# Optimization experiments

Measured on AMD Instinct MI355X. Metric: run time of the kernel, lower is better.

## Reference

```python
import jax, jax.numpy as jnp
import numpy as np

N_E = 1024
E_DIM = 256
BETA = 0.25
DECAY = 0.99
EPS = 1e-5


def setup_inputs() -> dict:
    key = jax.random.key(0)
    k1, k2 = jax.random.split(key)
    z = jax.random.normal(k1, (16, E_DIM, 64, 64), dtype=jnp.float32)
    # embedding.weight.data.uniform_(-1/n_e, 1/n_e)
    weight = jax.random.uniform(k2, (N_E, E_DIM), dtype=jnp.float32,
                                minval=-1.0 / N_E, maxval=1.0 / N_E)
    cluster_size = jnp.zeros((N_E,), dtype=jnp.float32)
    embedding_avg = weight  # clone of initial weight
    return {"z": z, "weight": weight, "cluster_size": cluster_size,
            "embedding_avg": embedding_avg}


def reference(z, weight, cluster_size, embedding_avg):
    B, C, H, W = z.shape  # C == e_dim
    zp = jnp.transpose(z, (0, 2, 3, 1))          # [B,H,W,C]
    zf = zp.reshape(-1, C)                       # [N, C], N = B*H*W

    # ||z||^2 + ||e||^2 - 2 z e^T  -> [N, n_e]
    d = (jnp.sum(zf * zf, axis=1, keepdims=True)
         + jnp.sum(weight * weight, axis=1)
         - 2.0 * jnp.matmul(zf, weight.T))
    idx = jnp.argmin(d, axis=1)                  # [N] int

    z_q = weight[idx].reshape(zp.shape)          # [B,H,W,C]

    # EMA codebook update (training branch), computed with scatter-sums
    n_e = weight.shape[0]
    counts = jax.ops.segment_sum(jnp.ones(zf.shape[0], dtype=zf.dtype),
                                 idx, num_segments=n_e)        # encodings.sum(0)
    new_cluster_size = cluster_size * DECAY + (1.0 - DECAY) * counts
    n = jnp.sum(new_cluster_size)
    cs_smoothed = (new_cluster_size + EPS) / (n + n_e * EPS) * n
    dw = jax.ops.segment_sum(zf, idx, num_segments=n_e)        # encodings.T @ zf
    new_embedding_avg = embedding_avg * DECAY + (1.0 - DECAY) * dw
    new_weight = new_embedding_avg / cs_smoothed[:, None]

    loss = BETA * jnp.mean((jax.lax.stop_gradient(z_q) - zp) ** 2)
    z_q_st = zp + jax.lax.stop_gradient(z_q - zp)   # straight-through
    out = jnp.transpose(z_q_st, (0, 3, 1, 2))        # back to NCHW
    return out, loss, idx, new_cluster_size, new_embedding_avg, new_weight
```

## Files before the change

### kernel.cpp

```cpp
#include <hip/hip_runtime.h>
#include <hip/hip_bf16.h>

typedef unsigned short ushort_t;
typedef __attribute__((ext_vector_type(8))) _Float16 half8;
typedef __attribute__((ext_vector_type(4))) _Float16 half4;
typedef __attribute__((ext_vector_type(4))) float f32x4;

#define NB    16
#define NC    256
#define NHW   4096
#define NPIX  65536
#define NE    1024
#define BETA  0.25f
#define DECAY 0.99f
#define EPS_  1e-5f
#define GAP_FLAG 1.25e-4f

#define OFF_LOSS 16777216
#define OFF_IDXF 16777217
#define OFF_NCS  16842753
#define OFF_NEA  16843777
#define OFF_NW   17105921

#define WS_WSUM  0
#define WS_CSSM  1024
#define WS_LPART 2048
#define WS_CNT   4096
#define WS_FLAGS 4128
#define WS_LIST  6176
#define WS_WF16  40960
#define WS_ZF16  (WS_WF16 + 131072)
#define WS_IDXI  (WS_ZF16 + 8388608)
#define WS_CCNT  (WS_IDXI + 65536)
#define WS_OFFS  (WS_CCNT + 1024)
#define WS_CUR   (WS_OFFS + 1024)
#define WS_SORT  (WS_CUR + 1024)
#define WS_END   (WS_SORT + 65536)

__device__ __forceinline__ float sq_nofma(float x) {
    float s = x * x;
    asm volatile("" : "+v"(s));
    return s;
}

__device__ __forceinline__ float np_pair128_sq(const float* __restrict__ a) {
    float r[8];
    #pragma unroll
    for (int m = 0; m < 8; ++m) r[m] = sq_nofma(a[m]);
    for (int i = 8; i < 128; i += 8) {
        #pragma unroll
        for (int m = 0; m < 8; ++m) r[m] += sq_nofma(a[i + m]);
    }
    return ((r[0] + r[1]) + (r[2] + r[3])) + ((r[4] + r[5]) + (r[6] + r[7]));
}

__device__ __forceinline__ void gload16(const void* g, void* ldsp) {
    __builtin_amdgcn_global_load_lds((const __attribute__((address_space(1))) unsigned int*)g,
                                     (__attribute__((address_space(3))) unsigned int*)ldsp,
                                     16, 0, 0);
}

__global__ __launch_bounds__(64) void wsum_kernel(const float* __restrict__ w,
                                                  float* __restrict__ wsum,
                                                  float* __restrict__ ncs,
                                                  int* __restrict__ cnt,
                                                  int* __restrict__ ccount,
                                                  float* __restrict__ lpart) {
    int j = blockIdx.x * 64 + threadIdx.x;
    const float* wr = w + (size_t)j * NC;
    wsum[j] = np_pair128_sq(wr) + np_pair128_sq(wr + 128);
    ncs[j] = 0.0f;
    ccount[j] = 0;
    lpart[j] = 0.0f;
    lpart[j + 1024] = 0.0f;
    if (j == 0) cnt[0] = 0;
}

__global__ __launch_bounds__(256) void wpack_kernel(const float* __restrict__ w,
                                                    _Float16* __restrict__ wf) {
    int i = blockIdx.x * 256 + threadIdx.x;
    wf[i] = (_Float16)(w[i] * 1024.0f);
}

__global__ __launch_bounds__(256) void zpack_kernel(const float* __restrict__ z,
                                                    _Float16* __restrict__ zf) {
    __shared__ float zs[64 * 65];
    const int t = threadIdx.x;
    const int P0 = blockIdx.x * 64;
    const int b = P0 >> 12, hw0 = P0 & (NHW - 1);
    const int K0 = blockIdx.y * 64;
    const int hw = t & 63, cq = t >> 6;
    const float* zb = z + (size_t)b * (NC * NHW) + hw0 + hw;
    #pragma unroll
    for (int i = 0; i < 16; ++i) {
        int kl = cq * 16 + i;
        zs[hw * 65 + kl] = zb[(size_t)(K0 + kl) * NHW];
    }
    __syncthreads();
    const int p = t >> 2, kq = t & 3;
    size_t obase = (size_t)(P0 + p) * NC + K0 + kq * 16;
    #pragma unroll
    for (int h2 = 0; h2 < 2; ++h2) {
        half8 v;
        #pragma unroll
        for (int j2 = 0; j2 < 8; ++j2)
            v[j2] = (_Float16)zs[p * 65 + kq * 16 + h2 * 8 + j2];
        *(half8*)&zf[obase + h2 * 8] = v;
    }
}

__global__ __launch_bounds__(512) void gemm2_kernel(const _Float16* __restrict__ wf,
                                                    const _Float16* __restrict__ zf,
                                                    const float* __restrict__ wsum,
                                                    float* __restrict__ idxf,
                                                    int* __restrict__ idxi,
                                                    ushort_t* __restrict__ list,
                                                    int* __restrict__ cnt,
                                                    float* __restrict__ ncs,
                                                    int* __restrict__ ccount) {
    __shared__ __align__(16) char smem[147456];
    _Float16* zt = (_Float16*)smem;
    _Float16* wt = (_Float16*)(smem + 131072);
    float* bvx = (float*)(smem + 131072);
    float* svx = bvx + 512;
    int*   bix = (int*)(svx + 512);
    int*   h   = (int*)smem;

    const int t = threadIdx.x;
    const int l = t & 63;
    const int w = t >> 6;
    const int P0 = blockIdx.x * 256;
    const int wc = w >> 2;
    const int wp = w & 3;

    const int sdest = w * 512 + l * 8;
    const int swrow = w * 16 + (l >> 2);
    const _Float16* wsrc0 = wf + (size_t)swrow * 256 + (((l & 3) ^ ((l >> 3) & 3)) * 8);
    int aoff[4];
    #pragma unroll
    for (int m = 0; m < 4; ++m) {
        int row = wc * 64 + m * 16 + (l & 15);
        int g = (l >> 4) ^ ((row >> 1) & 3);
        aoff[m] = row * 32 + g * 8;
    }
    int bbase[4], bx32[4];
    #pragma unroll
    for (int n = 0; n < 4; ++n) {
        int row = wp * 64 + n * 16 + (l & 15);
        int r3 = row & 7;
        bbase[n] = row * 256 + (((l >> 4) ^ (r3 & 3)) * 8);
        bx32[n] = (r3 >> 2) * 32;
    }

    #pragma unroll
    for (int i = 0; i < 16; ++i) {
        int row = w * 32 + i * 2 + (l >> 5);
        int gc = (l & 31) ^ (row & 7);
        gload16(zf + (size_t)(P0 + row) * NC + gc * 8,
                &zt[w * 8192 + i * 512 + l * 8]);
    }
    gload16(wsrc0, &wt[sdest]);

    float rbv2[4], rsv2[4];
    int   rbi2[4];
    #pragma unroll
    for (int n = 0; n < 4; ++n) { rbv2[n] = 3.4e38f; rsv2[n] = 3.4e38f; rbi2[n] = 0; }

    __syncthreads();

    for (int ct = 0; ct < 8; ++ct) {
        const _Float16* wsrc_ct = wsrc0 + ct * 32768;
        f32x4 acc[4][4];
        #pragma unroll
        for (int m = 0; m < 4; ++m)
            #pragma unroll
            for (int n = 0; n < 4; ++n)
                #pragma unroll
                for (int e = 0; e < 4; ++e) acc[m][n][e] = 0.0f;

        #pragma unroll
        for (int ks = 0; ks < 8; ++ks) {
            if (ct < 7 || ks < 7) {
                const _Float16* src = (ks < 7) ? (wsrc_ct + (ks + 1) * 32)
                                               : (wsrc_ct + 32768);
                gload16(src, &wt[((ks & 1) ^ 1) * 4096 + sdest]);
            }
            __builtin_amdgcn_s_setprio(1);
            half8 a[4], b[4];
            #pragma unroll
            for (int m = 0; m < 4; ++m)
                a[m] = *(const half8*)&wt[(ks & 1) * 4096 + aoff[m]];
            #pragma unroll
            for (int n = 0; n < 4; ++n)
                b[n] = *(const half8*)&zt[bbase[n] + ((ks * 32) ^ bx32[n])];
            #pragma unroll
            for (int m = 0; m < 4; ++m)
                #pragma unroll
                for (int n = 0; n < 4; ++n)
                    acc[m][n] = __builtin_amdgcn_mfma_f32_16x16x32_f16(a[m], b[n], acc[m][n], 0, 0, 0);
            __builtin_amdgcn_s_setprio(0);
            __syncthreads();
        }

        #pragma unroll
        for (int m = 0; m < 4; ++m) {
            float4 env = *(const float4*)&wsum[ct * 128 + wc * 64 + m * 16 + (l >> 4) * 4];
            const float* en = &env.x;
            #pragma unroll
            for (int n = 0; n < 4; ++n)
                #pragma unroll
                for (int r = 0; r < 4; ++r) {
                    float s = en[r] - acc[m][n][r] * 0.001953125f;
                    int code = ct * 128 + wc * 64 + m * 16 + (l >> 4) * 4 + r;
                    if (s < rbv2[n]) { rsv2[n] = rbv2[n]; rbv2[n] = s; rbi2[n] = code; }
                    else if (s < rsv2[n]) rsv2[n] = s;
                }
        }
    }

    #pragma unroll
    for (int n = 0; n < 4; ++n) {
        float bv = rbv2[n], sv = rsv2[n];
        int bi = rbi2[n];
        #pragma unroll
        for (int x = 16; x <= 32; x <<= 1) {
            float v2 = __shfl_xor(bv, x);
            float s2 = __shfl_xor(sv, x);
            int   i2 = __shfl_xor(bi, x);
            if (v2 < bv || (v2 == bv && i2 < bi)) { sv = fminf(bv, s2); bv = v2; bi = i2; }
            else sv = fminf(sv, v2);
        }
        if ((l >> 4) == 0) {
            int lp = wp * 64 + n * 16 + l;
            bvx[wc * 256 + lp] = bv;
            svx[wc * 256 + lp] = sv;
            bix[wc * 256 + lp] = bi;
        }
    }
    h[t] = 0;
    h[t + 512] = 0;
    __syncthreads();
    if (t < 256) {
        float bv = bvx[t], sv = svx[t];
        int bi = bix[t];
        float v2 = bvx[256 + t], s2 = svx[256 + t];
        int i2 = bix[256 + t];
        if (v2 < bv || (v2 == bv && i2 < bi)) { sv = fminf(bv, s2); bv = v2; bi = i2; }
        else sv = fminf(sv, v2);
        int pix = P0 + t;
        idxf[pix] = (float)bi;
        idxi[pix] = bi;
        atomicAdd(&h[bi], 1);
        if (sv - bv < GAP_FLAG) {
            int pos = atomicAdd(cnt, 1);
            list[pos] = (ushort_t)pix;
        }
    }
    __syncthreads();
    {
        int v = h[t];
        if (v) { atomicAdd(&ncs[t], (float)v); atomicAdd(&ccount[t], v); }
        v = h[t + 512];
        if (v) { atomicAdd(&ncs[t + 512], (float)v); atomicAdd(&ccount[t + 512], v); }
    }
}

__global__ __launch_bounds__(256) void argmin_kernel(const float* __restrict__ z,
                                                     const float* __restrict__ w,
                                                     const float* __restrict__ enorm,
                                                     float* __restrict__ idxf,
                                                     int* __restrict__ idxi,
                                                     unsigned long long* __restrict__ flags) {
    __shared__ __align__(16) float smem[64 * 68 + 128 * 68];
    float* zt = smem;
    float* wt = smem + 64 * 68;
    const int t = threadIdx.x;
    const int pr = t & 7;
    const int cr = t >> 3;
    const int P0 = blockIdx.x * 64;
    const int b = P0 >> 12;
    const int hw0 = P0 & (NHW - 1);
    const float* zb = z + (size_t)b * (NC * NHW) + hw0;
    float bestv[8], secv[8];
    int besti[8];
    #pragma unroll
    for (int i = 0; i < 8; ++i) { bestv[i] = 3.4e38f; secv[i] = 3.4e38f; besti[i] = 0; }
    for (int cc = 0; cc < 8; ++cc) {
        float acc[8][4];
        #pragma unroll
        for (int i = 0; i < 8; ++i)
            #pragma unroll
            for (int j = 0; j < 4; ++j) acc[i][j] = 0.0f;
        for (int kc = 0; kc < 4; ++kc) {
            {
                int p = t & 63;
                int k0 = (t >> 6) * 16;
                int f2 = ((p >> 3) & 3) << 2;
                #pragma unroll
                for (int i = 0; i < 16; ++i) {
                    int k = k0 + i;
                    zt[p * 68 + (k ^ f2)] = zb[(size_t)(kc * 64 + k) * NHW + p];
                }
            }
            {
                #pragma unroll
                for (int i = 0; i < 8; ++i) {
                    int f = t + 256 * i;
                    int jj = f >> 4;
                    int k4 = f & 15;
                    float4 v = *(const float4*)&w[(size_t)(cc * 128 + jj) * NC + kc * 64 + k4 * 4];
                    *(float4*)&wt[jj * 68 + k4 * 4] = v;
                }
            }
            __syncthreads();
            #pragma unroll 2
            for (int k = 0; k < 64; k += 4) {
                float4 za[8], wb[4];
                #pragma unroll
                for (int i = 0; i < 8; ++i)
                    za[i] = *(float4*)&zt[(pr + 8 * i) * 68 + (k ^ ((i & 3) << 2))];
                #pragma unroll
                for (int j = 0; j < 4; ++j)
                    wb[j] = *(float4*)&wt[(cr + 32 * j) * 68 + k];
                #pragma unroll
                for (int i = 0; i < 8; ++i)
                    #pragma unroll
                    for (int j = 0; j < 4; ++j)
                        acc[i][j] += za[i].x * wb[j].x + za[i].y * wb[j].y +
                                     za[i].z * wb[j].z + za[i].w * wb[j].w;
            }
            __syncthreads();
        }
        #pragma unroll
        for (int j = 0; j < 4; ++j) {
            int code = cc * 128 + cr + 32 * j;
            float enj = enorm[code];
            #pragma unroll
            for (int i = 0; i < 8; ++i) {
                float s = enj - 2.0f * acc[i][j];
                if (s < bestv[i]) { secv[i] = bestv[i]; bestv[i] = s; besti[i] = code; }
                else if (s < secv[i]) secv[i] = s;
            }
        }
    }
    float* rv = smem;
    int* ri = (int*)(smem + 2048);
    float* rs = smem + 4096;
    #pragma unroll
    for (int i = 0; i < 8; ++i) {
        int p = pr + 8 * i;
        rv[p * 32 + cr] = bestv[i];
        ri[p * 32 + cr] = besti[i];
        rs[p * 32 + cr] = secv[i];
    }
    __syncthreads();
    if (t < 64) {
        int p = t;
        float bv = rv[p * 32], sv = rs[p * 32];
        int bi = ri[p * 32];
        for (int s2 = 1; s2 < 32; ++s2) {
            float v = rv[p * 32 + s2];
            float v2 = rs[p * 32 + s2];
            int ii = ri[p * 32 + s2];
            if (v < bv) { sv = bv; bv = v; bi = ii; }
            else {
                if (v < sv) sv = v;
                if (v == bv && ii < bi) bi = ii;
            }
            if (v2 < sv) sv = v2;
        }
        idxf[P0 + p] = (float)bi;
        idxi[P0 + p] = bi;
        unsigned long long mask = __ballot((sv - bv) < GAP_FLAG);
        if (t == 0) flags[blockIdx.x] = mask;
    }
}

__global__ __launch_bounds__(256) void gather_kernel(const unsigned long long* __restrict__ flags,
                                                     ushort_t* __restrict__ list,
                                                     int* __restrict__ cnt) {
    int p = blockIdx.x * 256 + threadIdx.x;
    unsigned long long m = flags[p >> 6];
    if ((m >> (p & 63)) & 1ULL) {
        int pos = atomicAdd(cnt, 1);
        list[pos] = (ushort_t)p;
    }
}

__global__ __launch_bounds__(1024) void hist_kernel(const int* __restrict__ idxi,
                                                    float* __restrict__ ncs) {
    __shared__ int h[NE];
    int t = threadIdx.x;
    h[t] = 0;
    __syncthreads();
    int gid = blockIdx.x * 1024 + t;
    #pragma unroll
    for (int i = 0; i < 4; ++i) atomicAdd(&h[idxi[gid + i * 16384]], 1);
    __syncthreads();
    if (h[t]) atomicAdd(&ncs[t], (float)h[t]);
}

__global__ __launch_bounds__(1024, 8) void dwloss_kernel(const float* __restrict__ z,
                                                         const float* __restrict__ w,
                                                         const int* __restrict__ idxi,
                                                         float* __restrict__ dw0,
                                                         float* __restrict__ dw1,
                                                         float* __restrict__ lpart) {
    __shared__ float acc[NE];
    __shared__ float wcol[NE];
    __shared__ float ls[16];
    const int c = blockIdx.x;
    const int part = blockIdx.y;
    const int t = threadIdx.x;
    acc[t] = 0.0f;
    wcol[t] = w[(size_t)t * NC + c];
    __syncthreads();
    const float* zc = z + (size_t)c * NHW;
    float lsum = 0.0f;
    #pragma unroll
    for (int half = 0; half < 2; ++half) {
        float4 zv[4];
        int4   iv[4];
        #pragma unroll
        for (int i = 0; i < 4; ++i) {
            int b = part * 8 + half * 4 + i;
            zv[i] = *(const float4*)&zc[(size_t)b * (NC * NHW) + t * 4];
            iv[i] = *(const int4*)&idxi[b * 4096 + t * 4];
        }
        #pragma unroll
        for (int i = 0; i < 4; ++i) {
            float q0 = wcol[iv[i].x], q1 = wcol[iv[i].y];
            float q2 = wcol[iv[i].z], q3 = wcol[iv[i].w];
            float d0 = q0 - zv[i].x, d1 = q1 - zv[i].y;
            float d2 = q2 - zv[i].z, d3 = q3 - zv[i].w;
            lsum += d0 * d0 + d1 * d1 + d2 * d2 + d3 * d3;
            atomicAdd(&acc[iv[i].x], zv[i].x);
            atomicAdd(&acc[iv[i].y], zv[i].y);
            atomicAdd(&acc[iv[i].z], zv[i].z);
            atomicAdd(&acc[iv[i].w], zv[i].w);
        }
    }
    #pragma unroll
    for (int off = 32; off > 0; off >>= 1) lsum += __shfl_down(lsum, off);
    if ((t & 63) == 0) ls[t >> 6] = lsum;
    __syncthreads();
    if (t == 0) {
        float s = 0.0f;
        #pragma unroll
        for (int q = 0; q < 16; ++q) s += ls[q];
        lpart[c * 2 + part] = s;
    }
    float* dwp = part ? dw1 : dw0;
    dwp[(size_t)t * NC + c] = acc[t];
}

__global__ __launch_bounds__(256) void fixup3_kernel(const float* __restrict__ z,
                                                     const float* __restrict__ w,
                                                     const float* __restrict__ wsum,
                                                     const ushort_t* __restrict__ list,
                                                     const int* __restrict__ cnt,
                                                     float* __restrict__ idxf,
                                                     int* __restrict__ idxi,
                                                     float* __restrict__ ncs,
                                                     int* __restrict__ ccount) {
    const int count = cnt[0];
    if (count == 0) return;
    const int ngroups = (count + 7) >> 3;
    const int t = threadIdx.x;

    __shared__ __align__(16) char smem_raw[16384 + 8192];
    double (*zd)[NC] = (double(*)[NC])smem_raw;
    float  (*zf)[NC] = (float(*)[NC])(smem_raw + 16384);
    float* rbv = (float*)(smem_raw + 16384);
    int*   rbi = (int*)smem_raw;
    __shared__ float zs_sh[8];
    __shared__ int   pix_sh[8];
    __shared__ float r2v[8][32];
    __shared__ int   r2i[8][32];

    for (int g = blockIdx.x; g < ngroups; g += gridDim.x) {
        if (t < 8) {
            int i = g * 8 + t;
            pix_sh[t] = (i < count) ? (int)list[i] : (int)list[0];
        }
        __syncthreads();
        #pragma unroll
        for (int px = 0; px < 8; ++px) {
            int p = pix_sh[px];
            int b = p >> 12, hw = p & (NHW - 1);
            float zv = z[(size_t)b * (NC * NHW) + (size_t)t * NHW + hw];
            zf[px][t] = zv;
            zd[px][t] = (double)zv;
        }
        __syncthreads();
        if (t < 8) zs_sh[t] = np_pair128_sq(zf[t]) + np_pair128_sq(zf[t] + 128);
        __syncthreads();

        float zs_reg[8];
        #pragma unroll
        for (int px = 0; px < 8; ++px) zs_reg[px] = zs_sh[px];

        float bvr[8];
        int   bir[8];
        #pragma unroll
        for (int px = 0; px < 8; ++px) { bvr[px] = 3.4e38f; bir[px] = 0; }

        #pragma unroll
        for (int jo = 0; jo < 2; ++jo) {
            const int j0 = t + jo * 512;
            const int j1 = j0 + 256;
            const float* wr0 = w + (size_t)j0 * NC;
            const float* wr1 = w + (size_t)j1 * NC;
            double acc0[8], acc1[8];
            #pragma unroll
            for (int px = 0; px < 8; ++px) { acc0[px] = 0.0; acc1[px] = 0.0; }
            for (int k = 0; k < NC; k += 4) {
                float4 wa = *(const float4*)&wr0[k];
                float4 wb = *(const float4*)&wr1[k];
                const float* wap = (const float*)&wa;
                const float* wbp = (const float*)&wb;
                #pragma unroll
                for (int e = 0; e < 4; ++e) {
                    double wea = (double)wap[e];
                    double web = (double)wbp[e];
                    #pragma unroll
                    for (int px = 0; px < 8; ++px) {
                        double zv = zd[px][k + e];
                        acc0[px] += wea * zv;
                        acc1[px] += web * zv;
                    }
                }
            }
            float ws0 = wsum[j0], ws1 = wsum[j1];
            #pragma unroll
            for (int px = 0; px < 8; ++px) {
                float m0 = (float)acc0[px];
                float s10 = zs_reg[px] + ws0;
                float d0 = s10 - 2.0f * m0;
                if (d0 < bvr[px] || (d0 == bvr[px] && j0 < bir[px])) { bvr[px] = d0; bir[px] = j0; }
                float m1 = (float)acc1[px];
                float s11 = zs_reg[px] + ws1;
                float d1 = s11 - 2.0f * m1;
                if (d1 < bvr[px] || (d1 == bvr[px] && j1 < bir[px])) { bvr[px] = d1; bir[px] = j1; }
            }
        }
        __syncthreads();
        #pragma unroll
        for (int px = 0; px < 8; ++px) {
            rbv[px * 256 + t] = bvr[px];
            rbi[px * 256 + t] = bir[px];
        }
        __syncthreads();
        {
            int px = t >> 5, s = t & 31;
            float bv = rbv[px * 256 + s * 8];
            int   bi = rbi[px * 256 + s * 8];
            #pragma unroll
            for (int e = 1; e < 8; ++e) {
                float v2 = rbv[px * 256 + s * 8 + e];
                int   i2 = rbi[px * 256 + s * 8 + e];
                if (v2 < bv || (v2 == bv && i2 < bi)) { bv = v2; bi = i2; }
            }
            r2v[px][s] = bv;
            r2i[px][s] = bi;
        }
        __syncthreads();
        if (t < 8) {
            float bv = r2v[t][0];
            int   bi = r2i[t][0];
            for (int s = 1; s < 32; ++s) {
                float v2 = r2v[t][s];
                int   i2 = r2i[t][s];
                if (v2 < bv || (v2 == bv && i2 < bi)) { bv = v2; bi = i2; }
            }
            if (g * 8 + t < count) {
                int p = pix_sh[t];
                int old = idxi[p];
                if (old != bi) {
                    idxf[p] = (float)bi;
                    idxi[p] = bi;
                    atomicAdd(&ncs[old], -1.0f);
                    atomicAdd(&ncs[bi], 1.0f);
                    if (ccount) {
                        atomicAdd(&ccount[old], -1);
                        atomicAdd(&ccount[bi], 1);
                    }
                }
            }
        }
        __syncthreads();
    }
}

__global__ __launch_bounds__(1024, 8) void out2_kernel(const float* __restrict__ w,
                                                       const int* __restrict__ idxi,
                                                       float* __restrict__ outq) {
    __shared__ float wcol[NE];
    const int c = blockIdx.x;
    const int part = blockIdx.y;
    const int t = threadIdx.x;
    wcol[t] = w[(size_t)t * NC + c];
    __syncthreads();
    float* oc = outq + (size_t)c * NHW;
    #pragma unroll
    for (int half = 0; half < 2; ++half) {
        int4 iv[4];
        #pragma unroll
        for (int i = 0; i < 4; ++i) {
            int b = part * 8 + half * 4 + i;
            iv[i] = *(const int4*)&idxi[b * 4096 + t * 4];
        }
        asm volatile("" :: "v"(iv[0].x), "v"(iv[1].x), "v"(iv[2].x), "v"(iv[3].x));
        #pragma unroll
        for (int i = 0; i < 4; ++i) {
            int b = part * 8 + half * 4 + i;
            float4 ov;
            ov.x = wcol[iv[i].x]; ov.y = wcol[iv[i].y];
            ov.z = wcol[iv[i].z]; ov.w = wcol[iv[i].w];
            *(float4*)&oc[(size_t)b * (NC * NHW) + t * 4] = ov;
        }
    }
}

__global__ __launch_bounds__(1024) void scan_kernel(const int* __restrict__ ccount,
                                                    int* __restrict__ offs,
                                                    int* __restrict__ cur) {
    __shared__ int s[1024];
    int t = threadIdx.x;
    int c0 = ccount[t];
    s[t] = c0;
    __syncthreads();
    for (int off = 1; off < 1024; off <<= 1) {
        int v = (t >= off) ? s[t - off] : 0;
        __syncthreads();
        s[t] += v;
        __syncthreads();
    }
    int ex = s[t] - c0;
    offs[t] = ex;
    cur[t] = ex;
}

__global__ __launch_bounds__(256) void scatter2_kernel(const int* __restrict__ idxi,
                                                       int* __restrict__ cur,
                                                       int* __restrict__ sorted) {
    int p = blockIdx.x * 256 + threadIdx.x;
    int id = idxi[p];
    int pos = atomicAdd(&cur[id], 1);
    sorted[pos] = p;
}

__global__ __launch_bounds__(256) void dwsum2_kernel(const _Float16* __restrict__ zf,
                                                     const float* __restrict__ w,
                                                     const int* __restrict__ sorted,
                                                     const int* __restrict__ offs,
                                                     const int* __restrict__ ccount,
                                                     float* __restrict__ dw0,
                                                     float* __restrict__ dw1,
                                                     float* __restrict__ lpart) {
    const int t = threadIdx.x, l = t & 63, wv = t >> 6;
    const int j = blockIdx.x * 4 + wv;
    const int part = blockIdx.y;
    const float4 q = *(const float4*)&w[(size_t)j * NC + l * 4];
    const int start = offs[j], cntj = ccount[j];
    const int h0 = (cntj + 1) >> 1;
    const int s = part ? start + h0 : start;
    const int e = part ? start + cntj : start + h0;
    float a0 = 0.f, a1 = 0.f, a2 = 0.f, a3 = 0.f, lsum = 0.f;
    for (int base = s; base < e; base += 64) {
        int pm = (base + l < e) ? sorted[base + l] : 0;
        int nn = min(64, e - base);
        for (int i = 0; i < nn; ++i) {
            int p = __shfl(pm, i);
            half4 zv = *(const half4*)&zf[(size_t)p * NC + l * 4];
            float z0 = (float)zv[0], z1 = (float)zv[1];
            float z2 = (float)zv[2], z3 = (float)zv[3];
            a0 += z0; a1 += z1; a2 += z2; a3 += z3;
            float d0 = q.x - z0, d1 = q.y - z1, d2 = q.z - z2, d3 = q.w - z3;
            lsum += d0 * d0 + d1 * d1 + d2 * d2 + d3 * d3;
        }
    }
    float* dwp = part ? dw1 : dw0;
    float4 av = make_float4(a0, a1, a2, a3);
    *(float4*)&dwp[(size_t)j * NC + l * 4] = av;
    #pragma unroll
    for (int off = 32; off > 0; off >>= 1) lsum += __shfl_down(lsum, off);
    if (l == 0) lpart[j * 2 + part] = lsum;
}

__global__ __launch_bounds__(1024) void finalize_kernel(const float* __restrict__ cs,
                                                        const float* __restrict__ lpart,
                                                        float* __restrict__ ncs,
                                                        float* __restrict__ cssm,
                                                        float* __restrict__ loss) {
    int t = threadIdx.x;
    float cnt = ncs[t];
    float v = cs[t] * DECAY + (1.0f - DECAY) * cnt;
    ncs[t] = v;
    __shared__ float red[1024];
    red[t] = v;
    __syncthreads();
    for (int s = 512; s > 0; s >>= 1) {
        if (t < s) red[t] += red[t + s];
        __syncthreads();
    }
    float n = red[0];
    __syncthreads();
    cssm[t] = (v + EPS_) / (n + (float)NE * EPS_) * n;
    red[t] = lpart[t] + lpart[t + 1024];
    __syncthreads();
    for (int s = 512; s > 0; s >>= 1) {
        if (t < s) red[t] += red[t + s];
        __syncthreads();
    }
    if (t == 0) loss[0] = BETA * red[0] / 16777216.0f;
}

__global__ __launch_bounds__(256) void neaw_kernel(const float* __restrict__ ea,
                                                   const float* __restrict__ cssm,
                                                   float* __restrict__ nea,
                                                   float* __restrict__ nw) {
    int lin = blockIdx.x * 256 + threadIdx.x;
    float dw = nea[lin] + nw[lin];
    float v = DECAY * ea[lin] + (1.0f - DECAY) * dw;
    nea[lin] = v;
    nw[lin] = v / cssm[lin >> 8];
}

extern "C" void kernel_launch(void* const* d_in, const int* in_sizes, int n_in,
                              void* d_out, int out_size, void* d_ws, size_t ws_size,
                              hipStream_t stream) {
    const float* z  = (const float*)d_in[0];
    const float* w  = (const float*)d_in[1];
    const float* cs = (const float*)d_in[2];
    const float* ea = (const float*)d_in[3];

    float* out  = (float*)d_out;
    float* loss = out + OFF_LOSS;
    float* idxf = out + OFF_IDXF;
    float* ncs  = out + OFF_NCS;
    float* nea  = out + OFF_NEA;
    float* nw   = out + OFF_NW;

    float* wsf = (float*)d_ws;
    float* wsum = wsf + WS_WSUM;
    float* cssm = wsf + WS_CSSM;
    float* lpart = wsf + WS_LPART;
    int* cnt = (int*)(wsf + WS_CNT);
    unsigned long long* flags = (unsigned long long*)(wsf + WS_FLAGS);
    ushort_t* list = (ushort_t*)(wsf + WS_LIST);
    int* idxi = (int*)(wsf + WS_IDXI);
    int* ccount = (int*)(wsf + WS_CCNT);
    int* offs = (int*)(wsf + WS_OFFS);
    int* cur = (int*)(wsf + WS_CUR);
    int* sorted = (int*)(wsf + WS_SORT);

    const bool fast = ws_size >= (size_t)WS_END * 4;

    hipLaunchKernelGGL(wsum_kernel, dim3(16), dim3(64), 0, stream, w, wsum, ncs, cnt,
                       fast ? ccount : cnt, lpart);

    if (fast) {
        _Float16* wf16 = (_Float16*)(wsf + WS_WF16);
        _Float16* zf16 = (_Float16*)(wsf + WS_ZF16);
        hipLaunchKernelGGL(wpack_kernel, dim3(1024), dim3(256), 0, stream, w, wf16);
        hipLaunchKernelGGL(zpack_kernel, dim3(1024, 4), dim3(256), 0, stream, z, zf16);
        hipLaunchKernelGGL(gemm2_kernel, dim3(256), dim3(512), 0, stream,
                           wf16, zf16, wsum, idxf, idxi, list, cnt, ncs, ccount);
        hipLaunchKernelGGL(fixup3_kernel, dim3(256), dim3(256), 0, stream,
                           z, w, wsum, list, cnt, idxf, idxi, ncs, ccount);
        hipLaunchKernelGGL(out2_kernel, dim3(256, 2), dim3(1024), 0, stream, w, idxi, out);
        hipLaunchKernelGGL(scan_kernel, dim3(1), dim3(1024), 0, stream, ccount, offs, cur);
        hipLaunchKernelGGL(scatter2_kernel, dim3(256), dim3(256), 0, stream, idxi, cur, sorted);
        hipLaunchKernelGGL(dwsum2_kernel, dim3(256, 2), dim3(256), 0, stream,
                           zf16, w, sorted, offs, ccount, nea, nw, lpart);
    } else {
        hipLaunchKernelGGL(argmin_kernel, dim3(1024), dim3(256), 0, stream, z, w, wsum, idxf, idxi, flags);
        hipLaunchKernelGGL(gather_kernel, dim3(256), dim3(256), 0, stream, flags, list, cnt);
        hipLaunchKernelGGL(hist_kernel, dim3(16), dim3(1024), 0, stream, idxi, ncs);
        hipLaunchKernelGGL(fixup3_kernel, dim3(256), dim3(256), 0, stream,
                           z, w, wsum, list, cnt, idxf, idxi, ncs, (int*)nullptr);
        hipLaunchKernelGGL(out2_kernel, dim3(256, 2), dim3(1024), 0, stream, w, idxi, out);
        hipLaunchKernelGGL(dwloss_kernel, dim3(256, 2), dim3(1024), 0, stream, z, w, idxi, nea, nw, lpart);
    }

    hipLaunchKernelGGL(finalize_kernel, dim3(1), dim3(1024), 0, stream, cs, lpart, ncs, cssm, loss);
    hipLaunchKernelGGL(neaw_kernel, dim3(1024), dim3(256), 0, stream, ea, cssm, nea, nw);
}
```

Before: 260.0 us.

## Load codebook fragments directly from global into registers, drop LDS staging and barriers

Stops staging the fp16 codebook tiles through shared memory with per-k-step barriers. Each wave now loads its A fragments straight from global (L2-resident) into registers, double-buffered across k-steps. This removes the LDS round trip and the block-wide sync in the MFMA loop. In exchange, codebook loads are uncoalesced-ish and duplicated across the 4 wp waves, and more VGPRs are held by the register double buffer.

New measurement: 283.2 us. +8.9%, slower.

```diff
diff --git a/kernel.cpp b/kernel.cpp
--- a/kernel.cpp
+++ b/kernel.cpp
@@ -118,13 +118,10 @@
                                                     int* __restrict__ cnt,
                                                     float* __restrict__ ncs,
                                                     int* __restrict__ ccount) {
-    __shared__ __align__(16) char smem[147456];
-    _Float16* zt = (_Float16*)smem;
-    _Float16* wt = (_Float16*)(smem + 131072);
-    float* bvx = (float*)(smem + 131072);
-    float* svx = bvx + 512;
-    int*   bix = (int*)(svx + 512);
-    int*   h   = (int*)smem;
+    __shared__ __align__(16) _Float16 zt[256 * 256];
+    __shared__ float bvx[512], svx[512];
+    __shared__ int   bix[512];
+    __shared__ int   h[NE];
 
     const int t = threadIdx.x;
     const int l = t & 63;
@@ -133,16 +130,15 @@
     const int wc = w >> 2;
     const int wp = w & 3;
 
-    const int sdest = w * 512 + l * 8;
-    const int swrow = w * 16 + (l >> 2);
-    const _Float16* wsrc0 = wf + (size_t)swrow * 256 + (((l & 3) ^ ((l >> 3) & 3)) * 8);
-    int aoff[4];
-    #pragma unroll
-    for (int m = 0; m < 4; ++m) {
-        int row = wc * 64 + m * 16 + (l & 15);
-        int g = (l >> 4) ^ ((row >> 1) & 3);
-        aoff[m] = row * 32 + g * 8;
-    }
+    #pragma unroll
+    for (int i = 0; i < 16; ++i) {
+        int row = w * 32 + i * 2 + (l >> 5);
+        int gc = (l & 31) ^ (row & 7);
+        gload16(zf + (size_t)(P0 + row) * NC + gc * 8,
+                &zt[w * 8192 + i * 512 + l * 8]);
+    }
+
+    const _Float16* wbase = wf + ((wc * 64 + (l & 15)) * 256 + (l >> 4) * 8);
     int bbase[4], bx32[4];
     #pragma unroll
     for (int n = 0; n < 4; ++n) {
@@ -152,14 +148,9 @@
         bx32[n] = (r3 >> 2) * 32;
     }
 
-    #pragma unroll
-    for (int i = 0; i < 16; ++i) {
-        int row = w * 32 + i * 2 + (l >> 5);
-        int gc = (l & 31) ^ (row & 7);
-        gload16(zf + (size_t)(P0 + row) * NC + gc * 8,
-                &zt[w * 8192 + i * 512 + l * 8]);
-    }
-    gload16(wsrc0, &wt[sdest]);
+    half8 aA[4], aB[4];
+    #pragma unroll
+    for (int m = 0; m < 4; ++m) aA[m] = *(const half8*)(wbase + m * 4096);
 
     float rbv2[4], rsv2[4];
     int   rbi2[4];
@@ -168,8 +159,9 @@
 
     __syncthreads();
 
+    #pragma unroll 1
     for (int ct = 0; ct < 8; ++ct) {
-        const _Float16* wsrc_ct = wsrc0 + ct * 32768;
+        const _Float16* wct = wbase + ct * 32768;
         f32x4 acc[4][4];
         #pragma unroll
         for (int m = 0; m < 4; ++m)
@@ -179,27 +171,42 @@
                 for (int e = 0; e < 4; ++e) acc[m][n][e] = 0.0f;
 
         #pragma unroll
-        for (int ks = 0; ks < 8; ++ks) {
-            if (ct < 7 || ks < 7) {
-                const _Float16* src = (ks < 7) ? (wsrc_ct + (ks + 1) * 32)
-                                               : (wsrc_ct + 32768);
-                gload16(src, &wt[((ks & 1) ^ 1) * 4096 + sdest]);
-            }
-            __builtin_amdgcn_s_setprio(1);
-            half8 a[4], b[4];
-            #pragma unroll
-            for (int m = 0; m < 4; ++m)
-                a[m] = *(const half8*)&wt[(ks & 1) * 4096 + aoff[m]];
-            #pragma unroll
-            for (int n = 0; n < 4; ++n)
-                b[n] = *(const half8*)&zt[bbase[n] + ((ks * 32) ^ bx32[n])];
-            #pragma unroll
-            for (int m = 0; m < 4; ++m)
+        for (int kp = 0; kp < 4; ++kp) {
+            {
+                const _Float16* nsrc = wct + (2 * kp + 1) * 32;
+                #pragma unroll
+                for (int m = 0; m < 4; ++m) aB[m] = *(const half8*)(nsrc + m * 4096);
+                __builtin_amdgcn_s_setprio(1);
+                half8 b[4];
                 #pragma unroll
                 for (int n = 0; n < 4; ++n)
-                    acc[m][n] = __builtin_amdgcn_mfma_f32_16x16x32_f16(a[m], b[n], acc[m][n], 0, 0, 0);
-            __builtin_amdgcn_s_setprio(0);
-            __syncthreads();
+                    b[n] = *(const half8*)&zt[bbase[n] + (((2 * kp) * 32) ^ bx32[n])];
+                #pragma unroll
+                for (int m = 0; m < 4; ++m)
+                    #pragma unroll
+                    for (int n = 0; n < 4; ++n)
+                        acc[m][n] = __builtin_amdgcn_mfma_f32_16x16x32_f16(aA[m], b[n], acc[m][n], 0, 0, 0);
+                __builtin_amdgcn_s_setprio(0);
+            }
+            {
+                if (ct < 7 || kp < 3) {
+                    const _Float16* nsrc = (kp < 3) ? (wct + (2 * kp + 2) * 32)
+                                                    : (wct + 32768);
+                    #pragma unroll
+                    for (int m = 0; m < 4; ++m) aA[m] = *(const half8*)(nsrc + m * 4096);
+                }
+                __builtin_amdgcn_s_setprio(1);
+                half8 b[4];
+                #pragma unroll
+                for (int n = 0; n < 4; ++n)
+                    b[n] = *(const half8*)&zt[bbase[n] + (((2 * kp + 1) * 32) ^ bx32[n])];
+                #pragma unroll
+                for (int m = 0; m < 4; ++m)
+                    #pragma unroll
+                    for (int n = 0; n < 4; ++n)
+                        acc[m][n] = __builtin_amdgcn_mfma_f32_16x16x32_f16(aB[m], b[n], acc[m][n], 0, 0, 0);
+                __builtin_amdgcn_s_setprio(0);
+            }
         }
 
         #pragma unroll
```
